# Kernel tuning notes

Hardware: AMD Instinct MI355X
Metric: run time of the kernel (lower is better)

## Reference

```python
import jax, jax.numpy as jnp
import numpy as np

N_NODES = 10000
N_EDGES = 256000
N_GRAPHS = 32
N_ELEM = 10
F = 64      # channel multiplicity of hidden irreps
L = 9       # (max_ell+1)^2, max_ell=2, component-normalized real SH
NB = 8      # num_bessel
HID = 16    # MLP_irreps dim of nonlinear readout
RMAX = 5.0
PCUT = 6    # num_polynomial_cutoff
AVG = 25.6  # avg_num_neighbors


def _sph(u):
    # real spherical harmonics, e3nn 'component' normalization (sum_m Y^2 = 2l+1)
    x, y, z = u[:, 0], u[:, 1], u[:, 2]
    s3 = 3.0 ** 0.5; s5 = 5.0 ** 0.5; s15 = 15.0 ** 0.5
    return jnp.stack([
        jnp.ones_like(x),
        s3 * x, s3 * y, s3 * z,
        s15 * x * y, s15 * y * z, 0.5 * s5 * (3.0 * z * z - 1.0),
        s15 * x * z, 0.5 * s15 * (x * x - y * y)], axis=-1)


def _radial(r):
    # Bessel basis * polynomial cutoff envelope (RadialEmbeddingBlock)
    n = jnp.arange(1, NB + 1, dtype=r.dtype)
    bess = np.sqrt(2.0 / RMAX) * jnp.sin(n * np.pi * r[:, None] / RMAX) / r[:, None]
    x = r / RMAX
    p = PCUT
    env = (1.0 - 0.5 * (p + 1) * (p + 2) * x ** p + p * (p + 2) * x ** (p + 1)
           - 0.5 * p * (p + 1) * x ** (p + 2)) * (x < 1.0)
    return bess * env[:, None]


def _rmlp(ef, W1, W2, W3, W4):
    h = jax.nn.silu(ef @ W1)
    h = jax.nn.silu(h @ W2)
    h = jax.nn.silu(h @ W3)
    return h @ W4


def _energy(positions, node_attrs, shifts, atomic_energies, W_embed,
            R1_W1, R1_W2, R1_W3, R1_W4, R2_W1, R2_W2, R2_W3, R2_W4,
            W_lin1, W_sc1, W_prod1, w_read1, W_lin2, W_sc2, W_prod2,
            W_r1, w_r2, edge_index, batch, num_graphs):
    snd, rcv = edge_index[0], edge_index[1]
    n_nodes = positions.shape[0]
    e = edge_index.shape[1]
    vec = positions[rcv] - positions[snd] + shifts  # edge gather
    r = jnp.sqrt(jnp.sum(vec * vec, axis=-1) + 1e-12)
    sh = _sph(vec / r[:, None])       # [E, L]
    ef = _radial(r)                   # [E, NB]
    node_e0 = node_attrs @ atomic_energies                          # [N]
    e0 = jax.ops.segment_sum(node_e0, batch, num_segments=num_graphs)
    h0 = node_attrs @ W_embed                                       # [N, F]
    # ---- interaction 1: gather -> per-edge radial-weighted SH tensor product -> scatter ----
    tw1 = _rmlp(ef, R1_W1, R1_W2, R1_W3, R1_W4).reshape(e, F, L)
    msg1 = h0[snd][:, :, None] * sh[:, None, :] * tw1               # [E, F, L]
    agg1 = jax.ops.segment_sum(msg1, rcv, num_segments=n_nodes) / AVG
    feats1 = jnp.einsum('nfl,lfg->ngl', agg1, W_lin1)               # per-l channel mix
    feats1 = feats1.at[:, :, 0].add(h0 @ W_sc1)                     # skip connection
    inv1 = jnp.sum(feats1 * feats1, axis=-1)                        # [N, F] invariants
    h1 = feats1 * (1.0 + inv1 @ W_prod1)[:, :, None]                # product basis (simplified)
    e1_node = h1[:, :, 0] @ w_read1                                 # linear readout
    e1 = jax.ops.segment_sum(e1_node, batch, num_segments=num_graphs)
    # ---- interaction 2 ----
    s1 = h1[:, :, 0]
    tw2 = _rmlp(ef, R2_W1, R2_W2, R2_W3, R2_W4).reshape(e, F, L)
    msg2 = s1[snd][:, :, None] * sh[:, None, :] * tw2               # [E, F, L]
    agg2 = jax.ops.segment_sum(msg2, rcv, num_segments=n_nodes) / AVG
    feats2 = jnp.einsum('nfl,lfg->ngl', agg2, W_lin2)
    feats2 = feats2.at[:, :, 0].add(s1 @ W_sc2)
    inv2 = jnp.sum(feats2 * feats2, axis=-1)
    h2 = feats2 * (1.0 + inv2 @ W_prod2)[:, :, None]
    e2_node = jax.nn.silu(h2[:, :, 0] @ W_r1) @ w_r2                # nonlinear readout
    e2 = jax.ops.segment_sum(e2_node, batch, num_segments=num_graphs)
    total_energy = e0 + e1 + e2
    node_energy = node_e0 + e1_node + e2_node
    node_feats_out = jnp.concatenate(
        [h1.reshape(n_nodes, -1), h2.reshape(n_nodes, -1)], axis=-1)
    return total_energy, node_energy, node_feats_out


def setup_inputs() -> dict:
    key = jax.random.key(0)
    ks = jax.random.split(key, 24)
    w = lambda k, shape, fan: jax.random.normal(k, shape, dtype=jnp.float32) / np.sqrt(fan)
    positions = jax.random.normal(ks[0], (N_NODES, 3), dtype=jnp.float32) * 3.0
    elem = jax.random.randint(ks[1], (N_NODES,), 0, N_ELEM)
    node_attrs = jax.nn.one_hot(elem, N_ELEM, dtype=jnp.float32)
    edge_index = jax.random.randint(ks[2], (2, N_EDGES), 0, N_NODES)
    shifts = jnp.zeros((N_EDGES, 3), dtype=jnp.float32)
    batch = jnp.sort(jax.random.randint(ks[3], (N_NODES,), 0, N_GRAPHS))
    return {
        'positions': positions,
        'node_attrs': node_attrs,
        'shifts': shifts,
        'atomic_energies': jax.random.normal(ks[4], (N_ELEM,), dtype=jnp.float32),
        'W_embed': w(ks[5], (N_ELEM, F), N_ELEM),
        'R1_W1': w(ks[6], (NB, 64), NB), 'R1_W2': w(ks[7], (64, 64), 64),
        'R1_W3': w(ks[8], (64, 64), 64), 'R1_W4': w(ks[9], (64, F * L), 64),
        'R2_W1': w(ks[10], (NB, 64), NB), 'R2_W2': w(ks[11], (64, 64), 64),
        'R2_W3': w(ks[12], (64, 64), 64), 'R2_W4': w(ks[13], (64, F * L), 64),
        'W_lin1': w(ks[14], (L, F, F), F), 'W_sc1': w(ks[15], (F, F), F),
        'W_prod1': w(ks[16], (F, F), F), 'w_read1': w(ks[17], (F,), F),
        'W_lin2': w(ks[18], (L, F, F), F), 'W_sc2': w(ks[19], (F, F), F),
        'W_prod2': w(ks[20], (F, F), F),
        'W_r1': w(ks[21], (F, HID), F), 'w_r2': w(ks[22], (HID,), HID),
        'edge_index': edge_index,
        'batch': batch,
        'num_graphs': N_GRAPHS,
    }


def reference(positions, node_attrs, shifts, atomic_energies, W_embed,
              R1_W1, R1_W2, R1_W3, R1_W4, R2_W1, R2_W2, R2_W3, R2_W4,
              W_lin1, W_sc1, W_prod1, w_read1, W_lin2, W_sc2, W_prod2,
              W_r1, w_r2, edge_index, batch, num_graphs):
    args = (node_attrs, shifts, atomic_energies, W_embed,
            R1_W1, R1_W2, R1_W3, R1_W4, R2_W1, R2_W2, R2_W3, R2_W4,
            W_lin1, W_sc1, W_prod1, w_read1, W_lin2, W_sc2, W_prod2,
            W_r1, w_r2, edge_index, batch, num_graphs)
    total_energy, node_energy, node_feats_out = _energy(positions, *args)
    # forces = -dE/dpositions (compute_force=True path of MACE forward)
    forces = -jax.grad(lambda p: jnp.sum(_energy(p, *args)[0]))(positions)
    return (total_energy, node_energy, forces, node_feats_out)
```

## Files before the change

### kernel.cpp

```cpp
#include <hip/hip_runtime.h>
#include <cstddef>

#define NNODES 10000
#define NEDGES 256000
#define NGRAPH 32
#define NELEM  10
#define FF     64
#define LL     9
#define NBB    8
#define HIDN   16
#define RMAXF  5.0f
#define INV_AVG 0.0390625f
#define PI_F   3.14159265358979f
#define ECAP   98304
#define LSTR   640000

constexpr size_t O_H0    = 0;
constexpr size_t O_S1    = 640000;
constexpr size_t O_AGG1  = 1280000;
constexpr size_t O_AGG2  = 7040000;
constexpr size_t O_F1    = 12800000;
constexpr size_t O_F2    = 18560000;
constexpr size_t O_C1    = 24320000;
constexpr size_t O_C2    = 24960000;
constexpr size_t O_DS1   = 25600000;
constexpr size_t O_DINV  = 26240000;
constexpr size_t O_DH0C  = 26880000;
constexpr size_t O_CSH   = 27520000;
constexpr size_t O_CEF   = 28404736;
constexpr size_t O_CR    = 29191168;
constexpr size_t O_CVEC  = 29289472;
constexpr size_t O_DVEC  = 29584384;
constexpr size_t O_DPOS  = 29879296;
constexpr size_t O_CSND  = 29909296;
constexpr size_t O_CRCV  = 30007600;
constexpr size_t O_HIST  = 30105904;
constexpr size_t O_CURS  = 30115904;
constexpr size_t O_CNT   = 30125905;
constexpr size_t O_W4P1  = 30125920;
constexpr size_t O_W4P2  = 30175072;

__device__ __forceinline__ float siluf(float z){
  return z*(1.f/(1.f+__expf(-z)));
}
__device__ __forceinline__ float wred(float v){
#pragma unroll
  for(int o=32;o>0;o>>=1) v += __shfl_xor(v,o,64);
  return v;
}

__global__ __launch_bounds__(256) void k_w4prep(
    const float* __restrict__ W4a, const float* __restrict__ W4b,
    float* __restrict__ W4Pa, float* __restrict__ W4Pb){
  int o = blockIdx.x*256 + threadIdx.x;
  int which = (o >= 49152) ? 1 : 0;
  int oo = o - which*49152;
  int l = oo % 12;
  int fj = oo / 12;
  int ff = fj & 63;
  int j  = fj >> 6;
  const float* src = which ? W4b : W4a;
  float v = (l < 9) ? src[j*576 + ff*9 + l] : 0.f;
  (which ? W4Pb : W4Pa)[oo] = v;
}

__global__ __launch_bounds__(256) void k_embed(
    const float* __restrict__ attrs, const float* __restrict__ Wemb,
    const float* __restrict__ ae, const int* __restrict__ batch,
    float* __restrict__ h0, float* __restrict__ totE, float* __restrict__ nodeE){
  int t = blockIdx.x*256 + threadIdx.x;
  int n = t >> 6, f = t & 63;
  float acc = 0.f;
#pragma unroll
  for(int k=0;k<NELEM;k++) acc += attrs[n*NELEM+k]*Wemb[k*FF+f];
  h0[(size_t)n*FF+f] = acc;
  if(f==0){
    float e0 = 0.f;
#pragma unroll
    for(int k=0;k<NELEM;k++) e0 += attrs[n*NELEM+k]*ae[k];
    nodeE[n] = e0;
    atomicAdd(&totE[batch[n]], e0);
  }
}

__global__ __launch_bounds__(256) void k_count(
    const float* __restrict__ pos, const float* __restrict__ shifts,
    const int* __restrict__ eidx, int* __restrict__ hist){
  int e = blockIdx.x*256 + threadIdx.x;
  int sn = eidx[e], rc = eidx[NEDGES + e];
  float vx = pos[rc*3+0]-pos[sn*3+0]+shifts[(size_t)e*3+0];
  float vy = pos[rc*3+1]-pos[sn*3+1]+shifts[(size_t)e*3+1];
  float vz = pos[rc*3+2]-pos[sn*3+2]+shifts[(size_t)e*3+2];
  float r2 = vx*vx+vy*vy+vz*vz+1e-12f;
  if(r2 < RMAXF*RMAXF) atomicAdd(&hist[rc], 1);
}

__global__ __launch_bounds__(1024) void k_scan(
    const int* __restrict__ hist, int* __restrict__ cursor, int* __restrict__ cnt){
  __shared__ int buf[1024];
  __shared__ int carryS;
  int t = threadIdx.x;
  if(t==0) carryS = 0;
  __syncthreads();
  for(int c=0;c<10;c++){
    int i = c*1024 + t;
    int v = (i<NNODES)? hist[i] : 0;
    buf[t]=v;
    __syncthreads();
    for(int off=1; off<1024; off<<=1){
      int x = (t>=off)? buf[t-off] : 0;
      __syncthreads();
      buf[t] += x;
      __syncthreads();
    }
    int incl = buf[t];
    int base = carryS;
    if(i<NNODES) cursor[i] = base + incl - v;
    __syncthreads();
    if(t==1023) carryS += buf[1023];
    __syncthreads();
  }
  if(t==0){
    int n = carryS;
    cnt[0] = n;
    cnt[1] = (n+31)&~31;
  }
}

__global__ __launch_bounds__(256) void k_scatter(
    const float* __restrict__ pos, const float* __restrict__ shifts, const int* __restrict__ eidx,
    int* __restrict__ cursor,
    float* __restrict__ csh, float* __restrict__ cef, float* __restrict__ cr,
    float* __restrict__ cvec, int* __restrict__ csnd, int* __restrict__ crcv){
  int e = blockIdx.x*256 + threadIdx.x;
  int sn = eidx[e], rc = eidx[NEDGES + e];
  float vx = pos[rc*3+0]-pos[sn*3+0]+shifts[(size_t)e*3+0];
  float vy = pos[rc*3+1]-pos[sn*3+1]+shifts[(size_t)e*3+1];
  float vz = pos[rc*3+2]-pos[sn*3+2]+shifts[(size_t)e*3+2];
  float r2 = vx*vx+vy*vy+vz*vz+1e-12f;
  if(r2 >= RMAXF*RMAXF) return;
  float r = sqrtf(r2);
  int i = atomicAdd(&cursor[rc], 1);
  csnd[i]=sn; crcv[i]=rc; cr[i]=r;
  cvec[(size_t)i*3+0]=vx; cvec[(size_t)i*3+1]=vy; cvec[(size_t)i*3+2]=vz;
  float inv = 1.f/r, x=vx*inv, y=vy*inv, z=vz*inv;
  const float s3=1.7320508f, s5=2.23606798f, s15=3.87298335f;
  float* sh = csh + (size_t)i*LL;
  sh[0]=1.f; sh[1]=s3*x; sh[2]=s3*y; sh[3]=s3*z; sh[4]=s15*x*y; sh[5]=s15*y*z;
  sh[6]=0.5f*s5*(3.f*z*z-1.f); sh[7]=s15*x*z; sh[8]=0.5f*s15*(x*x-y*y);
  float xr = r*(1.f/RMAXF);
  float x2=xr*xr, x4=x2*x2, x6=x4*x2, x7=x6*xr, x8=x7*xr;
  float env = 1.f - 28.f*x6 + 48.f*x7 - 21.f*x8;
  const float CB = 0.632455532f;
#pragma unroll
  for(int b=0;b<NBB;b++){
    float a = (b+1)*(PI_F/RMAXF);
    cef[(size_t)i*NBB+b] = CB*sinf(a*r)*inv*env;
  }
}

__global__ void k_pad(float* csh, float* cef, float* cr, float* cvec,
                      int* csnd, int* crcv, const int* cnt){
  int n = cnt[0];
  int nr = cnt[1];
  int i = n + threadIdx.x;
  if(i < nr){
    csnd[i]=0; crcv[i]=NNODES-1; cr[i]=1.f;
    cvec[(size_t)i*3+0]=0.f; cvec[(size_t)i*3+1]=0.f; cvec[(size_t)i*3+2]=1.f;
    for(int l=0;l<LL;l++) csh[(size_t)i*LL+l]=0.f;
    for(int b=0;b<NBB;b++) cef[(size_t)i*NBB+b]=0.f;
  }
}

__global__ __launch_bounds__(256,2) void k_edge_fwd(
    const float* __restrict__ csh, const float* __restrict__ cef,
    const int* __restrict__ csnd, const int* __restrict__ crcv, const int* __restrict__ cnt,
    const float* __restrict__ src,
    const float* __restrict__ W1, const float* __restrict__ W2,
    const float* __restrict__ W3, const float* __restrict__ W4P,
    float* __restrict__ agg){
  const int cnt32 = cnt[1];
  if((int)(blockIdx.x*32) >= cnt32) return;
  __shared__ float W1s[NBB*FF];
  __shared__ float Wbuf[FF*65];
  __shared__ float hA[32*FF], hB[32*FF];
  __shared__ float shs[32*LL], efs[32*NBB];
  __shared__ int   sndS[32], rcvS[32];
  const int t = threadIdx.x;
  const size_t e0 = (size_t)blockIdx.x*32;
  for(int i=t;i<NBB*FF;i+=256) W1s[i]=W1[i];
  for(int i4=t;i4<1024;i4+=256){
    int i=i4*4; const float4 v=*(const float4*)&W2[i];
    float* dst=&Wbuf[((i>>6)*65)+(i&63)];
    dst[0]=v.x; dst[1]=v.y; dst[2]=v.z; dst[3]=v.w;
  }
  for(int i=t;i<32*LL;i+=256) shs[i]=csh[e0*LL+i];
  for(int i=t;i<32*NBB;i+=256) efs[i]=cef[e0*NBB+i];
  if(t<32){ sndS[t]=csnd[e0+t]; rcvS[t]=crcv[e0+t]; }
  __syncthreads();
  const int w=t>>6, f=t&63;
#pragma unroll
  for(int i=0;i<8;i++){
    int e=w*8+i; float z=0.f;
#pragma unroll
    for(int b=0;b<NBB;b++) z += efs[e*NBB+b]*W1s[b*FF+f];
    hA[e*FF+f]=siluf(z);
  }
#pragma unroll
  for(int i=0;i<8;i++){
    int e=w*8+i; float z=0.f;
#pragma unroll
    for(int j4=0;j4<16;j4++){
      const float4 hv=*(const float4*)&hA[e*FF+j4*4];
      z += hv.x*Wbuf[(j4*4+0)*65+f];
      z += hv.y*Wbuf[(j4*4+1)*65+f];
      z += hv.z*Wbuf[(j4*4+2)*65+f];
      z += hv.w*Wbuf[(j4*4+3)*65+f];
    }
    hB[e*FF+f]=siluf(z);
  }
  __syncthreads();
  for(int i4=t;i4<1024;i4+=256){
    int i=i4*4; const float4 v=*(const float4*)&W3[i];
    float* dst=&Wbuf[((i>>6)*65)+(i&63)];
    dst[0]=v.x; dst[1]=v.y; dst[2]=v.z; dst[3]=v.w;
  }
  __syncthreads();
#pragma unroll
  for(int i=0;i<8;i++){
    int e=w*8+i; float z=0.f;
#pragma unroll
    for(int j4=0;j4<16;j4++){
      const float4 hv=*(const float4*)&hB[e*FF+j4*4];
      z += hv.x*Wbuf[(j4*4+0)*65+f];
      z += hv.y*Wbuf[(j4*4+1)*65+f];
      z += hv.z*Wbuf[(j4*4+2)*65+f];
      z += hv.w*Wbuf[(j4*4+3)*65+f];
    }
    hA[e*FF+f]=siluf(z);
  }
  float tw[8][9];
#pragma unroll
  for(int i=0;i<8;i++)
#pragma unroll
    for(int l=0;l<LL;l++) tw[i][l]=0.f;
  for(int jc=0;jc<16;jc++){
    float4 h4[8];
#pragma unroll
    for(int i=0;i<8;i++) h4[i]=*(const float4*)&hA[(w*8+i)*FF + jc*4];
#pragma unroll
    for(int j4=0;j4<4;j4++){
      const float* wp = W4P + (size_t)(jc*4+j4)*768 + f*12;
      const float4 wa=*(const float4*)wp;
      const float4 wb=*(const float4*)(wp+4);
      const float  w8=wp[8];
#pragma unroll
      for(int i=0;i<8;i++){
        const float h3=(j4==0)?h4[i].x:(j4==1)?h4[i].y:(j4==2)?h4[i].z:h4[i].w;
        tw[i][0]+=h3*wa.x; tw[i][1]+=h3*wa.y; tw[i][2]+=h3*wa.z; tw[i][3]+=h3*wa.w;
        tw[i][4]+=h3*wb.x; tw[i][5]+=h3*wb.y; tw[i][6]+=h3*wb.z; tw[i][7]+=h3*wb.w;
        tw[i][8]+=h3*w8;
      }
    }
  }
  float sv[8];
#pragma unroll
  for(int i=0;i<8;i++) sv[i] = src[(size_t)sndS[w*8+i]*FF + f];
  const bool leftStraddle  = (e0>0) && (crcv[e0-1] == rcvS[0]);
  const bool rightStraddle = ((int)(e0+32) < cnt32) && (crcv[e0+32] == rcvS[31]);
  float* msgL = hB;
#pragma unroll
  for(int l=0;l<LL;l++){
#pragma unroll
    for(int i=0;i<8;i++){
      int e=w*8+i;
      msgL[e*FF+f] = sv[i]*shs[e*LL+l]*tw[i][l]*INV_AVG;
    }
    __syncthreads();
#pragma unroll
    for(int s0=0;s0<8;s0++){
      int s = w*8+s0;
      int rc = rcvS[s];
      bool head = (s==0) || (rcvS[s-1]!=rc);
      if(head){
        int L=1;
        while(s+L<32 && rcvS[s+L]==rc) L++;
        float sum=0.f;
        for(int k=0;k<L;k++) sum += msgL[(s+k)*FF+f];
        bool atom = (s==0 && leftStraddle) || (s+L==32 && rightStraddle);
        float* ap = &agg[(size_t)l*LSTR + (size_t)rc*FF + f];
        if(atom) atomicAdd(ap, sum); else *ap = sum;
      }
    }
    __syncthreads();
  }
}

__global__ __launch_bounds__(256,2) void k_lin2(
    const float* __restrict__ agg, const float* __restrict__ Wlin,
    const float* __restrict__ src, const float* __restrict__ Wsc,
    float* __restrict__ feats){
  const int l    = blockIdx.y;
  const int base = blockIdx.x*32;
  __shared__ float Wl[FF*65];
  __shared__ float aS[32*FF];
  const int t=threadIdx.x, w=t>>6, g=t&63;
  for(int i=t;i<FF*FF;i+=256) Wl[(i>>6)*65+(i&63)] = Wlin[(size_t)l*FF*FF+i];
#pragma unroll
  for(int j=0;j<8;j++){
    int idx=t+j*256;
    int n = base + (idx>>6);
    aS[idx] = (n<NNODES)? agg[(size_t)l*LSTR + (size_t)n*FF + (idx&63)] : 0.f;
  }
  __syncthreads();
  float acc[8];
#pragma unroll
  for(int i=0;i<8;i++) acc[i]=0.f;
#pragma unroll 4
  for(int f4=0;f4<16;f4++){
    float w0=Wl[(f4*4+0)*65+g], w1=Wl[(f4*4+1)*65+g],
          w2=Wl[(f4*4+2)*65+g], w3=Wl[(f4*4+3)*65+g];
#pragma unroll
    for(int i=0;i<8;i++){
      const float4 v = *(const float4*)&aS[(w*8+i)*FF + f4*4];
      acc[i] += w0*v.x+w1*v.y+w2*v.z+w3*v.w;
    }
  }
  if(l==0){
    __syncthreads();
    for(int i=t;i<FF*FF;i+=256) Wl[(i>>6)*65+(i&63)] = Wsc[i];
#pragma unroll
    for(int j=0;j<8;j++){
      int idx=t+j*256;
      int n = base + (idx>>6);
      aS[idx] = (n<NNODES)? src[(size_t)n*FF + (idx&63)] : 0.f;
    }
    __syncthreads();
#pragma unroll 4
    for(int f4=0;f4<16;f4++){
      float w0=Wl[(f4*4+0)*65+g], w1=Wl[(f4*4+1)*65+g],
            w2=Wl[(f4*4+2)*65+g], w3=Wl[(f4*4+3)*65+g];
#pragma unroll
      for(int i=0;i<8;i++){
        const float4 v = *(const float4*)&aS[(w*8+i)*FF + f4*4];
        acc[i] += w0*v.x+w1*v.y+w2*v.z+w3*v.w;
      }
    }
  }
#pragma unroll
  for(int i=0;i<8;i++){
    int n = base + w*8 + i;
    if(n<NNODES) feats[(size_t)l*LSTR + (size_t)n*FF + g] = acc[i];
  }
}

template<int LAYER>
__global__ __launch_bounds__(256,2) void k_prod(
    const float* __restrict__ feats, const int* __restrict__ batch,
    const float* __restrict__ Wpr,
    const float* __restrict__ wread, const float* __restrict__ Wr1, const float* __restrict__ wr2,
    float* __restrict__ cbuf, float* __restrict__ s1out,
    float* __restrict__ nfeats, float* __restrict__ nodeE, float* __restrict__ totE){
  __shared__ float Wprs[FF*65];
  __shared__ float Wr1s[FF*HIDN];
  __shared__ float ivS[4][FF];
  const int t=threadIdx.x, w=t>>6, g=t&63;
  for(int i=t;i<FF*FF;i+=256) Wprs[(i>>6)*65+(i&63)]=Wpr[i];
  if(LAYER==2) for(int i=t;i<FF*HIDN;i+=256) Wr1s[i]=Wr1[i];
  __syncthreads();
  for(int k=0;k<2;k++){
    int n = blockIdx.x*8 + k*4 + w;
    if(n>=NNODES) continue;
    float fr[9]; float iv=0.f;
#pragma unroll
    for(int l=0;l<LL;l++){ fr[l]=feats[(size_t)l*LSTR + (size_t)n*FF + g]; iv+=fr[l]*fr[l]; }
    ivS[w][g]=iv;
    float c=1.f;
#pragma unroll
    for(int gg=0;gg<FF;gg++) c += ivS[w][gg]*Wprs[gg*65+g];
    cbuf[(size_t)n*FF+g]=c;
    float* nf = nfeats + (size_t)n*(2*FF*LL) + (LAYER==2?FF*LL:0) + g*LL;
#pragma unroll
    for(int l=0;l<LL;l++) nf[l]=fr[l]*c;
    float s0 = fr[0]*c;
    float epart;
    if(LAYER==1){
      s1out[(size_t)n*FF+g]=s0;
      epart = s0*wread[g];
    } else {
      ivS[w][g]=s0;
      epart=0.f;
      if(g<HIDN){
        float tt=0.f;
#pragma unroll
        for(int gg=0;gg<FF;gg++) tt += ivS[w][gg]*Wr1s[gg*HIDN+g];
        epart = siluf(tt)*wr2[g];
      }
    }
    float es = wred(epart);
    if(g==0){ nodeE[n]+=es; atomicAdd(&totE[batch[n]], es); }
  }
}

template<int LAYER>
__global__ __launch_bounds__(256,2) void k_node_bwd(
    const float* __restrict__ feats, const float* __restrict__ cbuf,
    const float* __restrict__ Wpr, const float* __restrict__ Wsc,
    const float* __restrict__ Wr1, const float* __restrict__ wr2,
    const float* __restrict__ wread, const float* __restrict__ ds1in,
    const float* __restrict__ Wlin,
    float* __restrict__ ds1out, float* __restrict__ dagg){
  __shared__ float WbufA[FF*65];
  __shared__ float WbufB[(LAYER==2)?FF*65:1];
  __shared__ float poolA[2048];
  __shared__ float dinvS[32*FF];
  __shared__ float dh0cS[32*FF];
  __shared__ float rowS[4][FF];
  __shared__ float dtS[4][HIDN];
  const int t=threadIdx.x, w=t>>6, g=t&63;
  const int base = blockIdx.x*32;
  for(int i=t;i<FF*FF;i+=256) WbufA[(i>>6)*65+(i&63)]=Wpr[i];
  if(LAYER==2){
    for(int i=t;i<FF*FF;i+=256) WbufB[(i>>6)*65+(i&63)]=Wsc[i];
    for(int i=t;i<FF*HIDN;i+=256){
      poolA[i]=Wr1[i];
      poolA[1024 + (i&15)*FF + (i>>4)]=Wr1[i];
    }
  }
  __syncthreads();
  for(int k=0;k<8;k++){
    int ni = k*4+w;
    int n  = base + ni;
    if(n>=NNODES) continue;
    float f0 = feats[(size_t)n*FF+g];
    float c  = cbuf[(size_t)n*FF+g];
    float dh0;
    if(LAYER==2){
      rowS[w][g] = f0*c;
      if(g<HIDN){
        float tt=0.f;
#pragma unroll
        for(int gg=0;gg<FF;gg++) tt += rowS[w][gg]*poolA[gg*HIDN+g];
        float sg = 1.f/(1.f+__expf(-tt));
        dtS[w][g] = sg*(1.f + tt*(1.f-sg))*wr2[g];
      }
      dh0=0.f;
#pragma unroll
      for(int h=0;h<HIDN;h++) dh0 += dtS[w][h]*poolA[1024 + h*FF + g];
    } else {
      dh0 = wread[g] + ds1in[(size_t)n*FF+g];
    }
    rowS[w][g] = dh0*f0;
    float dinv=0.f;
#pragma unroll
    for(int gg=0;gg<FF;gg++) dinv += rowS[w][gg]*WbufA[g*65+gg];
    dinvS[ni*FF+g]=dinv;
    dh0cS[ni*FF+g]=dh0*c;
    if(LAYER==2){
      rowS[w][g] = 2.f*dinv*f0 + dh0*c;
      float ds=0.f;
#pragma unroll
      for(int gg=0;gg<FF;gg++) ds += rowS[w][gg]*WbufB[g*65+gg];
      ds1out[(size_t)n*FF+g]=ds;
    }
  }
  __syncthreads();
  float* fS = poolA;
  for(int l=0;l<LL;l++){
    for(int i=t;i<FF*FF;i+=256) WbufA[(i>>6)*65+(i&63)]=Wlin[(size_t)l*FF*FF+i];
#pragma unroll
    for(int j=0;j<8;j++){
      int idx=t+j*256;
      int n = base + (idx>>6);
      float v=0.f;
      if(n<NNODES){
        float ft = feats[(size_t)l*LSTR+(size_t)n*FF+(idx&63)];
        v = 2.f*dinvS[idx]*ft;
        if(l==0) v += dh0cS[idx];
      }
      fS[idx]=v;
    }
    __syncthreads();
    float acc[8];
#pragma unroll
    for(int i=0;i<8;i++) acc[i]=0.f;
#pragma unroll 4
    for(int f4=0;f4<16;f4++){
      float w0=WbufA[g*65+f4*4+0], w1=WbufA[g*65+f4*4+1],
            w2=WbufA[g*65+f4*4+2], w3=WbufA[g*65+f4*4+3];
#pragma unroll
      for(int i=0;i<8;i++){
        const float4 v = *(const float4*)&fS[(w*8+i)*FF + f4*4];
        acc[i] += w0*v.x+w1*v.y+w2*v.z+w3*v.w;
      }
    }
#pragma unroll
    for(int i=0;i<8;i++){
      int n = base + w*8 + i;
      if(n<NNODES) dagg[(size_t)l*LSTR + (size_t)n*FF + g] = acc[i];
    }
    __syncthreads();
  }
}

template<int LAYER>
__global__ __launch_bounds__(256,2) void k_edge_bwd(
    const float* __restrict__ csh, const float* __restrict__ cef,
    const float* __restrict__ cr, const float* __restrict__ cvec,
    const int* __restrict__ csnd, const int* __restrict__ crcv, const int* __restrict__ cnt,
    const float* __restrict__ src,
    const float* __restrict__ W1, const float* __restrict__ W2,
    const float* __restrict__ W3, const float* __restrict__ W4,
    const float* __restrict__ dagg,
    float* __restrict__ ds1,
    float* __restrict__ dvec,
    float* __restrict__ dpos){
  if((int)(blockIdx.x*8) >= cnt[1]) return;
  __shared__ float W1s[NBB*FF];
  __shared__ float Wbuf[FF*65];
  __shared__ float hP[8*FF];
  __shared__ float hQ[8*FF];
  __shared__ float hR[8*FF];
  __shared__ float shs[8*LL], efs[8*NBB];
  __shared__ float redS[4*512];
  __shared__ float dh3S[4*2*64];
  __shared__ float W4c[2][4*576];
  __shared__ int sndS[8], rcvS[8];
  const int t=threadIdx.x, w=t>>6, f=t&63;
  const size_t e0=(size_t)blockIdx.x*8;
  const float4* W4v=(const float4*)W4;
  for(int i=t;i<NBB*FF;i+=256) W1s[i]=W1[i];
  for(int i4=t;i4<1024;i4+=256){
    int i=i4*4; const float4 v=*(const float4*)&W2[i];
    float* dst=&Wbuf[((i>>6)*65)+(i&63)];
    dst[0]=v.x; dst[1]=v.y; dst[2]=v.z; dst[3]=v.w;
  }
  if(t<8*LL)  shs[t]=csh[e0*LL+t];
  if(t<8*NBB) efs[t]=cef[e0*NBB+t];
  if(t<8){ sndS[t]=csnd[e0+t]; rcvS[t]=crcv[e0+t]; }
  __syncthreads();
  float sv[2], dtw[2][9];
  float z1r[2], z2r[2], z3r[2];
#pragma unroll
  for(int i=0;i<2;i++) sv[i]=src[(size_t)sndS[w*2+i]*FF+f];
#pragma unroll
  for(int i=0;i<2;i++){
    int le=w*2+i; int rc=rcvS[le];
#pragma unroll
    for(int l=0;l<LL;l++){
      float dm0=dagg[(size_t)l*LSTR+(size_t)rc*FF+f]*INV_AVG;
      dtw[i][l]=dm0*sv[i]*shs[le*LL+l];
    }
  }
#pragma unroll
  for(int i=0;i<2;i++){
    int le=w*2+i; float z=0.f;
#pragma unroll
    for(int b=0;b<NBB;b++) z += efs[le*NBB+b]*W1s[b*FF+f];
    z1r[i]=z; hP[le*FF+f]=siluf(z);
  }
#pragma unroll
  for(int i=0;i<2;i++){
    int le=w*2+i; float z=0.f;
#pragma unroll
    for(int j4=0;j4<16;j4++){
      const float4 hv=*(const float4*)&hP[le*FF+j4*4];
      z += hv.x*Wbuf[(j4*4+0)*65+f];
      z += hv.y*Wbuf[(j4*4+1)*65+f];
      z += hv.z*Wbuf[(j4*4+2)*65+f];
      z += hv.w*Wbuf[(j4*4+3)*65+f];
    }
    z2r[i]=z; hQ[le*FF+f]=siluf(z);
  }
  __syncthreads();
  for(int i4=t;i4<1024;i4+=256){
    int i=i4*4; const float4 v=*(const float4*)&W3[i];
    float* dst=&Wbuf[((i>>6)*65)+(i&63)];
    dst[0]=v.x; dst[1]=v.y; dst[2]=v.z; dst[3]=v.w;
  }
  for(int d4=t; d4<576; d4+=256) ((float4*)W4c[0])[d4] = W4v[d4];
  __syncthreads();
#pragma unroll
  for(int i=0;i<2;i++){
    int le=w*2+i; float z=0.f;
#pragma unroll
    for(int j4=0;j4<16;j4++){
      const float4 hv=*(const float4*)&hQ[le*FF+j4*4];
      z += hv.x*Wbuf[(j4*4+0)*65+f];
      z += hv.y*Wbuf[(j4*4+1)*65+f];
      z += hv.z*Wbuf[(j4*4+2)*65+f];
      z += hv.w*Wbuf[(j4*4+3)*65+f];
    }
    z3r[i]=z; hR[le*FF+f]=siluf(z);
  }
  float tw[2][9];
#pragma unroll
  for(int i=0;i<2;i++)
#pragma unroll
    for(int l=0;l<LL;l++) tw[i][l]=0.f;
  float* redW = redS + w*512;
  const int row=f>>3, seg=f&7;
  int cur=0;
  for(int jc=0;jc<16;jc++){
    if(jc<15){
      float* dst=(float*)W4c[cur^1];
      for(int d4=t; d4<576; d4+=256) ((float4*)dst)[d4] = W4v[(jc+1)*576 + d4];
    }
    const float* Wc = W4c[cur];
    float4 h3v[2];
    h3v[0]=*(const float4*)&hR[(w*2+0)*FF + jc*4];
    h3v[1]=*(const float4*)&hR[(w*2+1)*FF + jc*4];
    float p[4][2];
#pragma unroll
    for(int j4=0;j4<4;j4++){
      const float* wp = Wc + j4*576 + f*9;
      const float w0=wp[0], w1=wp[1], w2=wp[2], w3=wp[3], w4_=wp[4],
                  w5=wp[5], w6=wp[6], w7=wp[7], w8=wp[8];
#pragma unroll
      for(int i=0;i<2;i++){
        const float h3=(j4==0)?h3v[i].x:(j4==1)?h3v[i].y:(j4==2)?h3v[i].z:h3v[i].w;
        tw[i][0]+=h3*w0; tw[i][1]+=h3*w1; tw[i][2]+=h3*w2; tw[i][3]+=h3*w3;
        tw[i][4]+=h3*w4_; tw[i][5]+=h3*w5; tw[i][6]+=h3*w6; tw[i][7]+=h3*w7;
        tw[i][8]+=h3*w8;
        float pp=0.f;
        pp+=dtw[i][0]*w0; pp+=dtw[i][1]*w1; pp+=dtw[i][2]*w2; pp+=dtw[i][3]*w3;
        pp+=dtw[i][4]*w4_; pp+=dtw[i][5]*w5; pp+=dtw[i][6]*w6; pp+=dtw[i][7]*w7;
        pp+=dtw[i][8]*w8;
        p[j4][i]=pp;
      }
    }
#pragma unroll
    for(int j4=0;j4<4;j4++)
#pragma unroll
      for(int i=0;i<2;i++){
        int r=j4*2+i;
        redW[r*64 + (f ^ ((r*9)&63))] = p[j4][i];
      }
    {
      float s=0.f;
#pragma unroll
      for(int k=0;k<8;k++) s += redW[row*64 + ((seg*8+k) ^ ((row*9)&63))];
      s += __shfl_xor(s,1,64);
      s += __shfl_xor(s,2,64);
      s += __shfl_xor(s,4,64);
      if(seg==0) dh3S[w*128 + (row&1)*64 + jc*4 + (row>>1)] = s;
    }
    __syncthreads();
    cur ^= 1;
  }
  float dux[2], duy[2], duz[2];
#pragma unroll
  for(int i=0;i<2;i++){
    int le=w*2+i; int rc=rcvS[le];
    size_t eg=e0+le;
    float vx=cvec[eg*3+0], vy=cvec[eg*3+1], vz=cvec[eg*3+2];
    float invr=1.f/cr[eg];
    float ux=vx*invr, uy=vy*invr, uz=vz*invr;
    const float s3=1.7320508f, s5=2.23606798f, s15=3.87298335f;
    float dm[9], d_[9];
#pragma unroll
    for(int l=0;l<LL;l++){
      dm[l]=dagg[(size_t)l*LSTR+(size_t)rc*FF+f]*INV_AVG;
      d_[l]=dm[l]*sv[i]*tw[i][l];
    }
    float duxp = s3*d_[1] + s15*(uy*d_[4] + uz*d_[7] + ux*d_[8]);
    float duyp = s3*d_[2] + s15*(ux*d_[4] + uz*d_[5] - uy*d_[8]);
    float duzp = s3*d_[3] + s15*(uy*d_[5] + ux*d_[7]) + 3.f*s5*uz*d_[6];
    dux[i]=wred(duxp); duy[i]=wred(duyp); duz[i]=wred(duzp);
    if(LAYER==2){
      float A=0.f;
#pragma unroll
      for(int l=0;l<LL;l++) A += dm[l]*shs[le*LL+l]*tw[i][l];
      atomicAdd(&ds1[(size_t)sndS[le]*FF+f], A);
    }
  }
#pragma unroll
  for(int i=0;i<2;i++){
    int le=w*2+i;
    float dh3 = dh3S[w*128 + i*64 + f];
    float sg3 = 1.f/(1.f+__expf(-z3r[i]));
    hQ[le*FF+f] = dh3*sg3*(1.f + z3r[i]*(1.f-sg3));
  }
  float dz2r[2];
#pragma unroll
  for(int i=0;i<2;i++){
    int le=w*2+i; float dh2=0.f;
#pragma unroll
    for(int c4=0;c4<16;c4++){
      const float4 dv=*(const float4*)&hQ[le*FF+c4*4];
      dh2 += dv.x*Wbuf[f*65+c4*4+0];
      dh2 += dv.y*Wbuf[f*65+c4*4+1];
      dh2 += dv.z*Wbuf[f*65+c4*4+2];
      dh2 += dv.w*Wbuf[f*65+c4*4+3];
    }
    float sg2=1.f/(1.f+__expf(-z2r[i]));
    dz2r[i]=dh2*sg2*(1.f + z2r[i]*(1.f-sg2));
  }
  __syncthreads();
  for(int i4=t;i4<1024;i4+=256){
    int i=i4*4; const float4 v=*(const float4*)&W2[i];
    float* dst=&Wbuf[((i>>6)*65)+(i&63)];
    dst[0]=v.x; dst[1]=v.y; dst[2]=v.z; dst[3]=v.w;
  }
  __syncthreads();
#pragma unroll
  for(int i=0;i<2;i++){ int le=w*2+i; hQ[le*FF+f]=dz2r[i]; }
#pragma unroll
  for(int i=0;i<2;i++){
    int le=w*2+i;
    float dh1=0.f;
#pragma unroll
    for(int c4=0;c4<16;c4++){
      const float4 dv=*(const float4*)&hQ[le*FF+c4*4];
      dh1 += dv.x*Wbuf[f*65+c4*4+0];
      dh1 += dv.y*Wbuf[f*65+c4*4+1];
      dh1 += dv.z*Wbuf[f*65+c4*4+2];
      dh1 += dv.w*Wbuf[f*65+c4*4+3];
    }
    float sg1=1.f/(1.f+__expf(-z1r[i]));
    float dz1=dh1*sg1*(1.f + z1r[i]*(1.f-sg1));
    size_t eg=e0+le;
    float r=cr[eg];
    float invr=1.f/r;
    float vx=cvec[eg*3+0], vy=cvec[eg*3+1], vz=cvec[eg*3+2];
    float ux=vx*invr, uy=vy*invr, uz=vz*invr;
    float xr=r*(1.f/RMAXF);
    float x2=xr*xr, x4=x2*x2, x5=x4*xr, x6=x5*xr, x7=x6*xr;
    float env=1.f-28.f*x6+48.f*x7-21.f*x7*xr;
    float envd=(-168.f*x5+336.f*x6-168.f*x7)*(1.f/RMAXF);
    const float CB=0.632455532f;
    float B=0.f;
#pragma unroll
    for(int b=0;b<NBB;b++){
      float a=(b+1)*(PI_F/RMAXF);
      float ar=a*r;
      float sn_=__sinf(ar), cs_=__cosf(ar);
      float bess=CB*sn_*invr;
      float bessd=(ar<1e-2f)?(-CB*a*a*a*r*(1.f/3.f)):(CB*(a*cs_-sn_*invr)*invr);
      B += W1s[b*FF+f]*(bessd*env + bess*envd);
    }
    float dr = wred(dz1*B);
    float udd=ux*dux[i]+uy*duy[i]+uz*duz[i];
    float dvx=dr*ux+(dux[i]-ux*udd)*invr;
    float dvy=dr*uy+(duy[i]-uy*udd)*invr;
    float dvz=dr*uz+(duz[i]-uz*udd)*invr;
    if(f==0){
      if(LAYER==2){
        dvec[eg*3+0]=dvx; dvec[eg*3+1]=dvy; dvec[eg*3+2]=dvz;
      } else {
        int sn=sndS[le], rc=rcvS[le];
        float tx=dvec[eg*3+0]+dvx, ty=dvec[eg*3+1]+dvy, tz=dvec[eg*3+2]+dvz;
        atomicAdd(&dpos[rc*3+0],tx); atomicAdd(&dpos[rc*3+1],ty); atomicAdd(&dpos[rc*3+2],tz);
        atomicAdd(&dpos[sn*3+0],-tx); atomicAdd(&dpos[sn*3+1],-ty); atomicAdd(&dpos[sn*3+2],-tz);
      }
    }
  }
}

__global__ __launch_bounds__(256) void k_forces(const float* __restrict__ dpos,
                                                float* __restrict__ forces){
  int i = blockIdx.x*256+threadIdx.x;
  if(i < NNODES*3) forces[i] = -dpos[i];
}

extern "C" void kernel_launch(void* const* d_in, const int* in_sizes, int n_in,
                              void* d_out, int out_size, void* d_ws, size_t ws_size,
                              hipStream_t stream){
  (void)in_sizes; (void)n_in; (void)out_size; (void)ws_size;
  const float* pos    = (const float*)d_in[0];
  const float* attrs  = (const float*)d_in[1];
  const float* shifts = (const float*)d_in[2];
  const float* ae     = (const float*)d_in[3];
  const float* Wemb   = (const float*)d_in[4];
  const float* R1W1   = (const float*)d_in[5];
  const float* R1W2   = (const float*)d_in[6];
  const float* R1W3   = (const float*)d_in[7];
  const float* R1W4   = (const float*)d_in[8];
  const float* R2W1   = (const float*)d_in[9];
  const float* R2W2   = (const float*)d_in[10];
  const float* R2W3   = (const float*)d_in[11];
  const float* R2W4   = (const float*)d_in[12];
  const float* Wlin1  = (const float*)d_in[13];
  const float* Wsc1   = (const float*)d_in[14];
  const float* Wpr1   = (const float*)d_in[15];
  const float* wrd1   = (const float*)d_in[16];
  const float* Wlin2  = (const float*)d_in[17];
  const float* Wsc2   = (const float*)d_in[18];
  const float* Wpr2   = (const float*)d_in[19];
  const float* Wr1    = (const float*)d_in[20];
  const float* wr2    = (const float*)d_in[21];
  const int*   eidx   = (const int*)d_in[22];
  const int*   batch  = (const int*)d_in[23];

  float* out = (float*)d_out;
  float* ws  = (float*)d_ws;
  float* totE   = out;
  float* nodeE  = out + 32;
  float* forces = out + 10032;
  float* nfeats = out + 40032;

  float* h0   = ws + O_H0;
  float* s1   = ws + O_S1;
  float* agg1 = ws + O_AGG1;
  float* agg2 = ws + O_AGG2;
  float* f1   = ws + O_F1;
  float* f2   = ws + O_F2;
  float* c1   = ws + O_C1;
  float* c2   = ws + O_C2;
  float* ds1  = ws + O_DS1;
  float* csh  = ws + O_CSH;
  float* cef  = ws + O_CEF;
  float* crr  = ws + O_CR;
  float* cvec = ws + O_CVEC;
  float* dvec = ws + O_DVEC;
  float* dpos = ws + O_DPOS;
  int* csnd = (int*)(ws + O_CSND);
  int* crcv = (int*)(ws + O_CRCV);
  int* hist = (int*)(ws + O_HIST);
  int* curs = (int*)(ws + O_CURS);
  int* cnt  = (int*)(ws + O_CNT);
  float* w4p1 = ws + O_W4P1;
  float* w4p2 = ws + O_W4P2;
  float* dagg2 = agg1;
  float* dagg1 = agg2;

  hipMemsetAsync(totE, 0, 32*sizeof(float), stream);
  hipMemsetAsync(agg1, 0, (size_t)2*5760000*sizeof(float), stream);
  hipMemsetAsync(dpos, 0, 30000*sizeof(float), stream);
  hipMemsetAsync(hist, 0, NNODES*sizeof(int), stream);

  dim3 gLin(313,9);

  k_w4prep<<<384,256,0,stream>>>(R1W4, R2W4, w4p1, w4p2);
  k_embed<<<2500,256,0,stream>>>(attrs, Wemb, ae, batch, h0, totE, nodeE);
  k_count<<<1000,256,0,stream>>>(pos, shifts, eidx, hist);
  k_scan<<<1,1024,0,stream>>>(hist, curs, cnt);
  k_scatter<<<1000,256,0,stream>>>(pos, shifts, eidx, curs, csh, cef, crr, cvec, csnd, crcv);
  k_pad<<<1,32,0,stream>>>(csh, cef, crr, cvec, csnd, crcv, cnt);

  k_edge_fwd<<<ECAP/32,256,0,stream>>>(csh,cef,csnd,crcv,cnt, h0,
                                       R1W1,R1W2,R1W3,w4p1, agg1);
  k_lin2<<<gLin,256,0,stream>>>(agg1, Wlin1, h0, Wsc1, f1);
  k_prod<1><<<1250,256,0,stream>>>(f1, batch, Wpr1, wrd1, nullptr, nullptr,
                                   c1, s1, nfeats, nodeE, totE);
  k_edge_fwd<<<ECAP/32,256,0,stream>>>(csh,cef,csnd,crcv,cnt, s1,
                                       R2W1,R2W2,R2W3,w4p2, agg2);
  k_lin2<<<gLin,256,0,stream>>>(agg2, Wlin2, s1, Wsc2, f2);
  k_prod<2><<<1250,256,0,stream>>>(f2, batch, Wpr2, nullptr, Wr1, wr2,
                                   c2, nullptr, nfeats, nodeE, totE);

  k_node_bwd<2><<<313,256,0,stream>>>(f2, c2, Wpr2, Wsc2, Wr1, wr2,
                                      nullptr, nullptr, Wlin2, ds1, dagg2);
  k_edge_bwd<2><<<ECAP/8,256,0,stream>>>(csh,cef,crr,cvec,csnd,crcv,cnt, s1,
                                         R2W1,R2W2,R2W3,R2W4, dagg2,
                                         ds1, dvec, nullptr);
  k_node_bwd<1><<<313,256,0,stream>>>(f1, c1, Wpr1, nullptr, nullptr, nullptr,
                                      wrd1, ds1, Wlin1, nullptr, dagg1);
  k_edge_bwd<1><<<ECAP/8,256,0,stream>>>(csh,cef,crr,cvec,csnd,crcv,cnt, h0,
                                         R1W1,R1W2,R1W3,R1W4, dagg1,
                                         nullptr, dvec, dpos);
  k_forces<<<118,256,0,stream>>>(dpos, forces);
}
```

Baseline: 2.323 ms.

## Shrink edge-backward LDS footprint by aliasing reduction and W4 buffers

Drops the dedicated reduction scratch and the double-buffered W4 chunk buffer from the edge-backward kernel. The W4 chunks and the per-wave reduction scratch now live in the existing Wbuf, hP and hQ arrays, and W3 is reloaded into Wbuf after the loop for the later gradient step. The goal is a much smaller shared-memory footprint so more blocks can be resident per CU. In exchange, the prefetch overlap of W4 chunks is lost and each chunk iteration gains an extra barrier plus a W3 reload.

```diff
diff --git a/kernel.cpp b/kernel.cpp
--- a/kernel.cpp
+++ b/kernel.cpp
@@ -516,15 +516,13 @@
     float* __restrict__ dvec,
     float* __restrict__ dpos){
   if((int)(blockIdx.x*8) >= cnt[1]) return;
-  __shared__ float W1s[NBB*FF];
-  __shared__ float Wbuf[FF*65];
-  __shared__ float hP[8*FF];
-  __shared__ float hQ[8*FF];
-  __shared__ float hR[8*FF];
+  __shared__ __align__(16) float W1s[NBB*FF];
+  __shared__ __align__(16) float Wbuf[FF*65];
+  __shared__ __align__(16) float hP[8*FF];
+  __shared__ __align__(16) float hQ[8*FF];
+  __shared__ __align__(16) float hR[8*FF];
   __shared__ float shs[8*LL], efs[8*NBB];
-  __shared__ float redS[4*512];
   __shared__ float dh3S[4*2*64];
-  __shared__ float W4c[2][4*576];
   __shared__ int sndS[8], rcvS[8];
   const int t=threadIdx.x, w=t>>6, f=t&63;
   const size_t e0=(size_t)blockIdx.x*8;
@@ -578,7 +576,6 @@
     float* dst=&Wbuf[((i>>6)*65)+(i&63)];
     dst[0]=v.x; dst[1]=v.y; dst[2]=v.z; dst[3]=v.w;
   }
-  for(int d4=t; d4<576; d4+=256) ((float4*)W4c[0])[d4] = W4v[d4];
   __syncthreads();
 #pragma unroll
   for(int i=0;i<2;i++){
@@ -593,27 +590,24 @@
     }
     z3r[i]=z; hR[le*FF+f]=siluf(z);
   }
+  __syncthreads();
   float tw[2][9];
 #pragma unroll
   for(int i=0;i<2;i++)
 #pragma unroll
     for(int l=0;l<LL;l++) tw[i][l]=0.f;
-  float* redW = redS + w*512;
+  float* redW = (w==0)? hP : (w==1)? hQ : &Wbuf[2304 + (w-2)*512];
   const int row=f>>3, seg=f&7;
-  int cur=0;
   for(int jc=0;jc<16;jc++){
-    if(jc<15){
-      float* dst=(float*)W4c[cur^1];
-      for(int d4=t; d4<576; d4+=256) ((float4*)dst)[d4] = W4v[(jc+1)*576 + d4];
-    }
-    const float* Wc = W4c[cur];
+    for(int d4=t; d4<576; d4+=256) ((float4*)Wbuf)[d4] = W4v[jc*576 + d4];
+    __syncthreads();
     float4 h3v[2];
     h3v[0]=*(const float4*)&hR[(w*2+0)*FF + jc*4];
     h3v[1]=*(const float4*)&hR[(w*2+1)*FF + jc*4];
     float p[4][2];
 #pragma unroll
     for(int j4=0;j4<4;j4++){
-      const float* wp = Wc + j4*576 + f*9;
+      const float* wp = Wbuf + j4*576 + f*9;
       const float w0=wp[0], w1=wp[1], w2=wp[2], w3=wp[3], w4_=wp[4],
                   w5=wp[5], w6=wp[6], w7=wp[7], w8=wp[8];
 #pragma unroll
@@ -646,7 +640,11 @@
       if(seg==0) dh3S[w*128 + (row&1)*64 + jc*4 + (row>>1)] = s;
     }
     __syncthreads();
-    cur ^= 1;
+  }
+  for(int i4=t;i4<1024;i4+=256){
+    int i=i4*4; const float4 v=*(const float4*)&W3[i];
+    float* dst=&Wbuf[((i>>6)*65)+(i&63)];
+    dst[0]=v.x; dst[1]=v.y; dst[2]=v.z; dst[3]=v.w;
   }
   float dux[2], duy[2], duz[2];
 #pragma unroll
@@ -674,6 +672,7 @@
       atomicAdd(&ds1[(size_t)sndS[le]*FF+f], A);
     }
   }
+  __syncthreads();
 #pragma unroll
   for(int i=0;i<2;i++){
     int le=w*2+i;
```

After: 2.385 ms. +2.6%, slower.
